# Performance work log

Hardware: AMD Instinct MI355X
Metric: run time of the kernel (lower is better)

The kernel has to match this reference:

```python
import jax, jax.numpy as jnp
import numpy as np

EMBED_DIM = 512
N_HEAD = 8
HEAD_DIM = EMBED_DIM // N_HEAD  # 64
B, S = 2, 4096
NEG_FILL = -1e20


def setup_inputs() -> dict:
    key = jax.random.key(0)
    ks = jax.random.split(key, 9)
    inp = {
        "key": jax.random.normal(ks[0], (B, S, EMBED_DIM), jnp.float32),
        "query": jax.random.normal(ks[1], (B, S, EMBED_DIM), jnp.float32),
        "value": jax.random.normal(ks[2], (B, S, EMBED_DIM), jnp.float32),
        "mask": jax.random.randint(ks[3], (1, 1, S, S), 0, 2, jnp.int32),
        # per-head projections (shared across heads, as in the source: a single
        # d x d nn.Linear applied to the last dim of [B,S,H,d])
        "Wq": jax.random.normal(ks[4], (HEAD_DIM, HEAD_DIM), jnp.float32) / np.sqrt(HEAD_DIM),
        "Wk": jax.random.normal(ks[5], (HEAD_DIM, HEAD_DIM), jnp.float32) / np.sqrt(HEAD_DIM),
        "Wv": jax.random.normal(ks[6], (HEAD_DIM, HEAD_DIM), jnp.float32) / np.sqrt(HEAD_DIM),
        "Wo": jax.random.normal(ks[7], (EMBED_DIM, EMBED_DIM), jnp.float32) / np.sqrt(EMBED_DIM),
        "bo": jax.random.normal(ks[8], (EMBED_DIM,), jnp.float32) * 0.01,
    }
    return inp


def reference(key, query, value, mask, Wq, Wk, Wv, Wo, bo):
    b, sq, e = query.shape
    skv = key.shape[1]
    h, d = N_HEAD, HEAD_DIM
    # split heads: [B, S, H, d]
    q = query.reshape(b, sq, h, d) @ Wq.T
    k = key.reshape(b, skv, h, d) @ Wk.T
    v = value.reshape(b, skv, h, d) @ Wv.T
    # scores: [B, H, Sq, Skv]
    scores = jnp.einsum("bqhd,bkhd->bhqk", q, k)
    # source masks BEFORE scaling: fill -1e20 then divide by sqrt(d)
    scores = jnp.where(mask == 0, NEG_FILL, scores)
    scores = scores / np.sqrt(d).astype(np.float32)
    attn = jax.nn.softmax(scores, axis=-1)
    ctx = jnp.einsum("bhqk,bkhd->bqhd", attn, v)  # [B, Sq, H, d]
    concat = ctx.reshape(b, sq, h * d)
    return concat @ Wo.T + bo
```

## Files before the change

kernel.cpp:

```cpp
#include <hip/hip_runtime.h>

typedef __bf16 bf16;
typedef __attribute__((ext_vector_type(8)))  bf16     bf16x8;
typedef __attribute__((ext_vector_type(4)))  bf16     bf16x4;
typedef __attribute__((ext_vector_type(16))) float    f32x16;
typedef __attribute__((ext_vector_type(4)))  float    f32x4;
typedef __attribute__((ext_vector_type(4)))  unsigned uint4v;
typedef __attribute__((ext_vector_type(2)))  unsigned uint2v;

#define SLEN 4096
#define NHEAD 8
#define HDIM 64
#define EMB 512
#define LOG2E 1.4426950408889634f
#define SCALE_LOG2E 0.1803336100254854f

__device__ __forceinline__ f32x16 mfma32(bf16x8 a, bf16x8 b, f32x16 c) {
  return __builtin_amdgcn_mfma_f32_32x32x16_bf16(a, b, c, 0, 0, 0);
}

__device__ __forceinline__ void cp16(const void* g, const void* l) {
  __builtin_amdgcn_global_load_lds(
      (__attribute__((address_space(1))) unsigned int*)(unsigned long long)g,
      (__attribute__((address_space(3))) unsigned int*)(unsigned int)(unsigned long long)l,
      16, 0, 0);
}

__device__ __forceinline__ unsigned pk2(float a, float b) {
  unsigned short ua = __builtin_bit_cast(unsigned short, (bf16)a);
  unsigned short ub = __builtin_bit_cast(unsigned short, (bf16)b);
  return (unsigned)ua | ((unsigned)ub << 16);
}

__global__ __launch_bounds__(256, 2) void proj_qkv(
    const float* __restrict__ key, const float* __restrict__ query, const float* __restrict__ value,
    const float* __restrict__ Wq, const float* __restrict__ Wk, const float* __restrict__ Wv,
    bf16* __restrict__ Qb, bf16* __restrict__ Kb, bf16* __restrict__ VT)
{
  __shared__ __align__(16) bf16 tile[128][64];
  const int tid = threadIdx.x, w = tid >> 6, lane = tid & 63, l31 = lane & 31, lh = lane >> 5;
  const int r0 = blockIdx.x * 128;
  const int m0 = r0 + w * 32;

  #pragma unroll
  for (int p = 0; p < 3; ++p) {
    const float* X = (p == 0) ? query : (p == 1) ? key : value;
    const float* W = (p == 0) ? Wq    : (p == 1) ? Wk  : Wv;

    bf16x8 af[4];
    {
      const float* xr = X + (size_t)(m0 + l31) * 64 + 8 * lh;
      #pragma unroll
      for (int c = 0; c < 4; ++c) {
        f32x4 lo = *(const f32x4*)(xr + c * 16);
        f32x4 hi = *(const f32x4*)(xr + c * 16 + 4);
        bf16x8 v;
        #pragma unroll
        for (int j = 0; j < 4; ++j) { v[j] = (bf16)lo[j]; v[4 + j] = (bf16)hi[j]; }
        af[c] = v;
      }
    }
    bf16x8 bfr[2][4];
    #pragma unroll
    for (int nb = 0; nb < 2; ++nb) {
      const float* wr = W + (size_t)(l31 + 32 * nb) * 64 + 8 * lh;
      #pragma unroll
      for (int c = 0; c < 4; ++c) {
        f32x4 lo = *(const f32x4*)(wr + c * 16);
        f32x4 hi = *(const f32x4*)(wr + c * 16 + 4);
        bf16x8 v;
        #pragma unroll
        for (int j = 0; j < 4; ++j) { v[j] = (bf16)lo[j]; v[4 + j] = (bf16)hi[j]; }
        bfr[nb][c] = v;
      }
    }
    f32x16 a0, a1;
    #pragma unroll
    for (int r = 0; r < 16; ++r) { a0[r] = 0.f; a1[r] = 0.f; }
    #pragma unroll
    for (int c = 0; c < 4; ++c) {
      a0 = mfma32(af[c], bfr[0][c], a0);
      a1 = mfma32(af[c], bfr[1][c], a1);
    }

    __syncthreads();
    #pragma unroll
    for (int r = 0; r < 16; ++r) {
      const int row = w * 32 + (r & 3) + 8 * (r >> 2) + 4 * lh;
      tile[row][l31]      = (bf16)a0[r];
      tile[row][l31 + 32] = (bf16)a1[r];
    }
    __syncthreads();

    if (p < 2) {
      bf16* OUT = p ? Kb : Qb;
      const int rloc = tid >> 1, half = tid & 1;
      const int rg = r0 + rloc, bs = rg >> 3, h = rg & 7, b = bs >> 12, sidx = bs & 4095;
      bf16* dst = OUT + (((size_t)(b * 8 + h) * SLEN + sidx) * 64 + half * 32);
      const bf16* srcp = &tile[rloc][half * 32];
      #pragma unroll
      for (int u = 0; u < 4; ++u) *(uint4v*)(dst + u * 8) = *(const uint4v*)(srcp + u * 8);
    } else {
      const int h = tid >> 5, d0 = tid & 31;
      const int b = blockIdx.x >> 8, s0 = (blockIdx.x * 16) & 4095;
      #pragma unroll
      for (int dh = 0; dh < 2; ++dh) {
        const int dd = d0 + 32 * dh;
        unsigned pk4[8];
        #pragma unroll
        for (int t2 = 0; t2 < 8; ++t2) {
          unsigned short ua = __builtin_bit_cast(unsigned short, tile[(2 * t2) * 8 + h][dd]);
          unsigned short ub = __builtin_bit_cast(unsigned short, tile[(2 * t2 + 1) * 8 + h][dd]);
          pk4[t2] = (unsigned)ua | ((unsigned)ub << 16);
        }
        bf16* dst = VT + ((size_t)(b * 8 + h) * 64 + dd) * SLEN + s0;
        uint4v A; A[0] = pk4[0]; A[1] = pk4[1]; A[2] = pk4[2]; A[3] = pk4[3];
        uint4v Bv; Bv[0] = pk4[4]; Bv[1] = pk4[5]; Bv[2] = pk4[6]; Bv[3] = pk4[7];
        *(uint4v*)(dst) = A;
        *(uint4v*)(dst + 8) = Bv;
      }
    }
  }
}

__global__ void pack_mask(const int* __restrict__ mask, unsigned long long* __restrict__ MBt)
{
  const int w = threadIdx.x >> 6, lane = threadIdx.x & 63;
  const int q = blockIdx.x * 4 + w;
  const int* row = mask + (size_t)q * SLEN;
  unsigned long long mine = 0ull;
  #pragma unroll 4
  for (int i = 0; i < 64; ++i) {
    unsigned long long b = __ballot(row[i * 64 + lane] != 0);
    if (i == lane) mine = b;
  }
  MBt[(size_t)lane * SLEN + q] = mine;
}

__global__ void wo_split(const float* __restrict__ Wo, bf16* __restrict__ WH, bf16* __restrict__ WL)
{
  const int i = (blockIdx.x * 256 + threadIdx.x) * 4;
  f32x4 v = *(const f32x4*)(Wo + i);
  bf16x4 h, l;
  #pragma unroll
  for (int j = 0; j < 4; ++j) { h[j] = (bf16)v[j]; l[j] = (bf16)(v[j] - (float)h[j]); }
  *(bf16x4*)(WH + i) = h;
  *(bf16x4*)(WL + i) = l;
}

__device__ __forceinline__ void stage_kv2(const bf16* Kb, const bf16* VT, bf16* Kf, bf16* Vf,
                                          int bh, int kv0, int buf, int w, int l31, int lh)
{
  #pragma unroll
  for (int qq = 0; qq < 4; ++qq) {
    const int fid = w * 4 + qq, mb = fid >> 2, c = fid & 3;
    const bf16* ks = Kb + ((size_t)bh * SLEN + kv0 + 32 * mb + l31) * HDIM + c * 16 + 8 * lh;
    cp16(ks, Kf + buf * 4096 + fid * 512);
    const bf16* vs = VT + ((size_t)bh * HDIM + 32 * mb + l31) * SLEN + kv0 + c * 16 + 8 * lh;
    cp16(vs, Vf + buf * 4096 + fid * 512);
  }
}

__global__ __launch_bounds__(128, 2) void attn_kernel(
    const bf16* __restrict__ Qb, const bf16* __restrict__ Kb, const bf16* __restrict__ VT,
    const unsigned long long* __restrict__ MBt,
    bf16* __restrict__ ctxh, bf16* __restrict__ ctxl)
{
  __shared__ __align__(16) unsigned char smem[32768];
  bf16* Kf = (bf16*)smem;
  bf16* Vf = (bf16*)(smem + 16384);

  const int tid = threadIdx.x, w = tid >> 6, lane = tid & 63, l31 = lane & 31, lh = lane >> 5;
  const int bh = blockIdx.x >> 6, qt = blockIdx.x & 63;
  const int q0 = qt * 64;
  const int qrow = q0 + w * 32 + l31;
  const int lh4 = 4 * lh;

  bf16x8 qf[4];
  {
    const bf16* qp = Qb + ((size_t)bh * SLEN + qrow) * HDIM + 8 * lh;
    #pragma unroll
    for (int c = 0; c < 4; ++c) qf[c] = *(const bf16x8*)(qp + c * 16);
  }

  f32x16 o0, o1;
  #pragma unroll
  for (int r = 0; r < 16; ++r) { o0[r] = 0.f; o1[r] = 0.f; }
  float ls0 = 0.f, ls1 = 0.f, ls2 = 0.f, ls3 = 0.f;

  stage_kv2(Kb, VT, Kf, Vf, bh, 0, 0, w, l31, lh);
  __syncthreads();

  unsigned long long mw = MBt[qrow];
  const int NT = SLEN / 64;
  for (int t = 0; t < NT; ++t) {
    const int cur = t & 1;
    if (t + 1 < NT) stage_kv2(Kb, VT, Kf, Vf, bh, (t + 1) * 64, cur ^ 1, w, l31, lh);
    unsigned long long mwn = 0ull;
    if (t + 1 < NT) mwn = MBt[(size_t)(t + 1) * SLEN + qrow];

    f32x16 s0, s1;
    #pragma unroll
    for (int r = 0; r < 16; ++r) { s0[r] = 0.f; s1[r] = 0.f; }
    #pragma unroll
    for (int c = 0; c < 4; ++c) {
      bf16x8 a0 = *(const bf16x8*)(Kf + cur * 4096 + c * 512 + lane * 8);
      bf16x8 a1 = *(const bf16x8*)(Kf + cur * 4096 + (4 + c) * 512 + lane * 8);
      s0 = mfma32(a0, qf[c], s0);
      s1 = mfma32(a1, qf[c], s1);
    }

    const unsigned wlo = (unsigned)mw, whi = (unsigned)(mw >> 32);
    float p0[16], p1[16];
    #pragma unroll
    for (int r = 0; r < 16; ++r) {
      const int sh = (r & 3) + 8 * (r >> 2) + lh4;
      float e0 = exp2f(s0[r] * SCALE_LOG2E);
      float e1 = exp2f(s1[r] * SCALE_LOG2E);
      e0 *= (float)((wlo >> sh) & 1u);
      e1 *= (float)((whi >> sh) & 1u);
      p0[r] = e0; p1[r] = e1;
      if ((r & 1) == 0) { ls0 += e0; ls1 += e1; } else { ls2 += e0; ls3 += e1; }
    }

    bf16x8 bp[4];
    #pragma unroll
    for (int mi = 0; mi < 2; ++mi) {
      #pragma unroll
      for (int cc = 0; cc < 2; ++cc) {
        const int rb = cc * 8;
        unsigned wA0 = pk2(mi ? p1[rb + 0] : p0[rb + 0], mi ? p1[rb + 1] : p0[rb + 1]);
        unsigned wA1 = pk2(mi ? p1[rb + 2] : p0[rb + 2], mi ? p1[rb + 3] : p0[rb + 3]);
        unsigned wB0 = pk2(mi ? p1[rb + 4] : p0[rb + 4], mi ? p1[rb + 5] : p0[rb + 5]);
        unsigned wB1 = pk2(mi ? p1[rb + 6] : p0[rb + 6], mi ? p1[rb + 7] : p0[rb + 7]);
        uint2v r0 = __builtin_amdgcn_permlane32_swap(wA0, wB0, false, false);
        uint2v r1 = __builtin_amdgcn_permlane32_swap(wA1, wB1, false, false);
        uint4v fw; fw[0] = r0[0]; fw[1] = r1[0]; fw[2] = r0[1]; fw[3] = r1[1];
        bp[2 * mi + cc] = __builtin_bit_cast(bf16x8, fw);
      }
    }

    #pragma unroll
    for (int c = 0; c < 4; ++c) {
      bf16x8 v0 = *(const bf16x8*)(Vf + cur * 4096 + c * 512 + lane * 8);
      bf16x8 v1 = *(const bf16x8*)(Vf + cur * 4096 + (4 + c) * 512 + lane * 8);
      o0 = mfma32(v0, bp[c], o0);
      o1 = mfma32(v1, bp[c], o1);
    }

    __syncthreads();
    mw = mwn;
  }

  float lsum = (ls0 + ls2) + (ls1 + ls3);
  lsum += __shfl_xor(lsum, 32);
  const float inv = 1.f / lsum;
  #pragma unroll
  for (int r = 0; r < 16; ++r) { o0[r] *= inv; o1[r] *= inv; }

  bf16* Tr = (bf16*)smem;
  const int rloc = tid >> 1, half = tid & 1;

  #pragma unroll
  for (int r = 0; r < 16; ++r) {
    const int dr = (r & 3) + 8 * (r >> 2) + lh4;
    Tr[(w * 32 + l31) * 72 + dr]      = (bf16)o0[r];
    Tr[(w * 32 + l31) * 72 + 32 + dr] = (bf16)o1[r];
  }
  __syncthreads();
  {
    bf16* dst = ctxh + ((size_t)bh * SLEN + q0 + rloc) * 64 + half * 32;
    const bf16* srcp = Tr + rloc * 72 + half * 32;
    #pragma unroll
    for (int u = 0; u < 4; ++u) *(uint4v*)(dst + u * 8) = *(const uint4v*)(srcp + u * 8);
  }
  __syncthreads();
  #pragma unroll
  for (int r = 0; r < 16; ++r) {
    const int dr = (r & 3) + 8 * (r >> 2) + lh4;
    const float h0 = (float)(bf16)o0[r];
    const float h1 = (float)(bf16)o1[r];
    Tr[(w * 32 + l31) * 72 + dr]      = (bf16)(o0[r] - h0);
    Tr[(w * 32 + l31) * 72 + 32 + dr] = (bf16)(o1[r] - h1);
  }
  __syncthreads();
  {
    bf16* dst = ctxl + ((size_t)bh * SLEN + q0 + rloc) * 64 + half * 32;
    const bf16* srcp = Tr + rloc * 72 + half * 32;
    #pragma unroll
    for (int u = 0; u < 4; ++u) *(uint4v*)(dst + u * 8) = *(const uint4v*)(srcp + u * 8);
  }
}

__global__ __launch_bounds__(256, 2) void out_proj(
    const bf16* __restrict__ CH, const bf16* __restrict__ CL,
    const bf16* __restrict__ WH, const bf16* __restrict__ WL,
    const float* __restrict__ bo, float* __restrict__ out)
{
  __shared__ __align__(16) bf16 Af[2][4][4][64][8];
  const int tid = threadIdx.x, w = tid >> 6, lane = tid & 63, l31 = lane & 31, lh = lane >> 5;
  const int mt = blockIdx.x >> 3, nt = blockIdx.x & 7;
  const int bs0 = mt * 128, n0 = nt * 64;
  const int b = bs0 >> 12, sbase = bs0 & 4095;

  f32x16 a0, a1;
  #pragma unroll
  for (int r = 0; r < 16; ++r) { a0[r] = 0.f; a1[r] = 0.f; }

  for (int kk = 0; kk < 8; ++kk) {
    __syncthreads();
    #pragma unroll
    for (int qq = 0; qq < 8; ++qq) {
      const int fid = w * 8 + qq, pl = fid >> 4, mb = (fid >> 2) & 3, c = fid & 3;
      const bf16* src = (pl ? CL : CH) +
          ((size_t)(b * 8 + kk) * SLEN + sbase + 32 * mb + l31) * 64 + 16 * c + 8 * lh;
      cp16(src, &Af[pl][mb][c][0][0]);
    }
    __syncthreads();

    bf16x8 bh0[4], bl0[4], bh1[4], bl1[4], ah[4], al[4];
    #pragma unroll
    for (int c = 0; c < 4; ++c) {
      const size_t o0off = (size_t)(n0 + l31) * EMB + kk * 64 + 16 * c + 8 * lh;
      const size_t o1off = (size_t)(n0 + l31 + 32) * EMB + kk * 64 + 16 * c + 8 * lh;
      bh0[c] = *(const bf16x8*)(WH + o0off);
      bl0[c] = *(const bf16x8*)(WL + o0off);
      bh1[c] = *(const bf16x8*)(WH + o1off);
      bl1[c] = *(const bf16x8*)(WL + o1off);
      ah[c] = *(const bf16x8*)(&Af[0][w][c][lane][0]);
      al[c] = *(const bf16x8*)(&Af[1][w][c][lane][0]);
    }
    #pragma unroll
    for (int c = 0; c < 4; ++c) {
      a0 = mfma32(ah[c], bh0[c], a0);
      a0 = mfma32(ah[c], bl0[c], a0);
      a0 = mfma32(al[c], bh0[c], a0);
      a1 = mfma32(ah[c], bh1[c], a1);
      a1 = mfma32(ah[c], bl1[c], a1);
      a1 = mfma32(al[c], bh1[c], a1);
    }
  }

  const float bv0 = bo[n0 + l31], bv1 = bo[n0 + l31 + 32];
  #pragma unroll
  for (int r = 0; r < 16; ++r) {
    const int row = bs0 + w * 32 + (r & 3) + 8 * (r >> 2) + 4 * lh;
    out[(size_t)row * EMB + n0 + l31]      = a0[r] + bv0;
    out[(size_t)row * EMB + n0 + l31 + 32] = a1[r] + bv1;
  }
}

extern "C" void kernel_launch(void* const* d_in, const int* in_sizes, int n_in,
                              void* d_out, int out_size, void* d_ws, size_t ws_size,
                              hipStream_t stream)
{
  (void)in_sizes; (void)n_in; (void)out_size; (void)ws_size;
  const float* key   = (const float*)d_in[0];
  const float* query = (const float*)d_in[1];
  const float* value = (const float*)d_in[2];
  const int*   mask  = (const int*)d_in[3];
  const float* Wq    = (const float*)d_in[4];
  const float* Wk    = (const float*)d_in[5];
  const float* Wv    = (const float*)d_in[6];
  const float* Wo    = (const float*)d_in[7];
  const float* bo    = (const float*)d_in[8];
  float* out = (float*)d_out;

  char* ws = (char*)d_ws;
  bf16* Qb = (bf16*)(ws);
  bf16* Kb = (bf16*)(ws + (8ull  << 20));
  bf16* VT = (bf16*)(ws + (16ull << 20));
  unsigned long long* MBp = (unsigned long long*)(ws + (24ull << 20));
  bf16* CH = (bf16*)(ws + (26ull << 20));
  bf16* CL = (bf16*)(ws + (34ull << 20));
  bf16* WH = (bf16*)(ws + (42ull << 20));
  bf16* WL = (bf16*)(ws + (42ull << 20) + (512ull << 10));

  proj_qkv<<<512, 256, 0, stream>>>(key, query, value, Wq, Wk, Wv, Qb, Kb, VT);
  pack_mask<<<1024, 256, 0, stream>>>(mask, MBp);
  wo_split<<<256, 256, 0, stream>>>(Wo, WH, WL);
  attn_kernel<<<1024, 128, 0, stream>>>(Qb, Kb, VT, MBp, CH, CL);
  out_proj<<<512, 256, 0, stream>>>(CH, CL, WH, WL, bo, out);
}
```

Measured before the change: 275.5 us.

## Split each KV tile across two extra waves per query group, reducing partials via LDS

The attention block grows from 2 to 4 waves. Each pair of waves handles one 32-row query group, and within the pair each wave takes half of every 64-key tile. Each wave now holds one score tile instead of two, which cuts its exp and packing work and register use per tile. The mask is repacked into two 32-bit words per 64-key tile, split by half-lane, so each wave can shift out its 16 mask bits directly. The trade-off is an extra LDS reduction of the partial outputs and softmax sums at the end. Occupancy is raised by using more waves per block.

```diff
diff --git a/kernel.cpp b/kernel.cpp
--- a/kernel.cpp
+++ b/kernel.cpp
@@ -12,7 +12,7 @@
 #define NHEAD 8
 #define HDIM 64
 #define EMB 512
-#define LOG2E 1.4426950408889634f
+#define NTILES 64
 #define SCALE_LOG2E 0.1803336100254854f
 
 __device__ __forceinline__ f32x16 mfma32(bf16x8 a, bf16x8 b, f32x16 c) {
@@ -123,7 +123,12 @@
   }
 }
 
-__global__ void pack_mask(const int* __restrict__ mask, unsigned long long* __restrict__ MBt)
+__device__ __forceinline__ unsigned nib_compress(unsigned x) {
+  x = (x | (x >> 4)) & 0x00FF00FFu;
+  x = (x | (x >> 8)) & 0x0000FFFFu;
+  return x;
+}
+__global__ void pack_mask(const int* __restrict__ mask, unsigned* __restrict__ MW)
 {
   const int w = threadIdx.x >> 6, lane = threadIdx.x & 63;
   const int q = blockIdx.x * 4 + w;
@@ -134,7 +139,11 @@
     unsigned long long b = __ballot(row[i * 64 + lane] != 0);
     if (i == lane) mine = b;
   }
-  MBt[(size_t)lane * SLEN + q] = mine;
+  const unsigned lo = (unsigned)mine, hi = (unsigned)(mine >> 32);
+  const unsigned w0 = nib_compress(lo & 0x0F0F0F0Fu)        | (nib_compress(hi & 0x0F0F0F0Fu) << 16);
+  const unsigned w1 = nib_compress((lo >> 4) & 0x0F0F0F0Fu) | (nib_compress((hi >> 4) & 0x0F0F0F0Fu) << 16);
+  MW[(size_t)lane * SLEN + q] = w0;
+  MW[(size_t)NTILES * SLEN + (size_t)lane * SLEN + q] = w1;
 }
 
 __global__ void wo_split(const float* __restrict__ Wo, bf16* __restrict__ WH, bf16* __restrict__ WL)
@@ -148,12 +157,12 @@
   *(bf16x4*)(WL + i) = l;
 }
 
-__device__ __forceinline__ void stage_kv2(const bf16* Kb, const bf16* VT, bf16* Kf, bf16* Vf,
+__device__ __forceinline__ void stage_kv4(const bf16* Kb, const bf16* VT, bf16* Kf, bf16* Vf,
                                           int bh, int kv0, int buf, int w, int l31, int lh)
 {
   #pragma unroll
-  for (int qq = 0; qq < 4; ++qq) {
-    const int fid = w * 4 + qq, mb = fid >> 2, c = fid & 3;
+  for (int qq = 0; qq < 2; ++qq) {
+    const int fid = w * 2 + qq, mb = fid >> 2, c = fid & 3;
     const bf16* ks = Kb + ((size_t)bh * SLEN + kv0 + 32 * mb + l31) * HDIM + c * 16 + 8 * lh;
     cp16(ks, Kf + buf * 4096 + fid * 512);
     const bf16* vs = VT + ((size_t)bh * HDIM + 32 * mb + l31) * SLEN + kv0 + c * 16 + 8 * lh;
@@ -161,9 +170,9 @@
   }
 }
 
-__global__ __launch_bounds__(128, 2) void attn_kernel(
+__global__ __launch_bounds__(256, 4) void attn_kernel(
     const bf16* __restrict__ Qb, const bf16* __restrict__ Kb, const bf16* __restrict__ VT,
-    const unsigned long long* __restrict__ MBt,
+    const unsigned* __restrict__ MW,
     bf16* __restrict__ ctxh, bf16* __restrict__ ctxl)
 {
   __shared__ __align__(16) unsigned char smem[32768];
@@ -171,9 +180,10 @@
   bf16* Vf = (bf16*)(smem + 16384);
 
   const int tid = threadIdx.x, w = tid >> 6, lane = tid & 63, l31 = lane & 31, lh = lane >> 5;
+  const int qg = w & 1, kc = w >> 1;
   const int bh = blockIdx.x >> 6, qt = blockIdx.x & 63;
   const int q0 = qt * 64;
-  const int qrow = q0 + w * 32 + l31;
+  const int qrow = q0 + qg * 32 + l31;
   const int lh4 = 4 * lh;
 
   bf16x8 qf[4];
@@ -188,103 +198,126 @@
   for (int r = 0; r < 16; ++r) { o0[r] = 0.f; o1[r] = 0.f; }
   float ls0 = 0.f, ls1 = 0.f, ls2 = 0.f, ls3 = 0.f;
 
-  stage_kv2(Kb, VT, Kf, Vf, bh, 0, 0, w, l31, lh);
-  __syncthreads();
-
-  unsigned long long mw = MBt[qrow];
-  const int NT = SLEN / 64;
-  for (int t = 0; t < NT; ++t) {
+  stage_kv4(Kb, VT, Kf, Vf, bh, 0, 0, w, l31, lh);
+  __syncthreads();
+
+  const unsigned* MWl = MW + (size_t)lh * NTILES * SLEN;
+  unsigned mw = MWl[qrow];
+  for (int t = 0; t < NTILES; ++t) {
     const int cur = t & 1;
-    if (t + 1 < NT) stage_kv2(Kb, VT, Kf, Vf, bh, (t + 1) * 64, cur ^ 1, w, l31, lh);
-    unsigned long long mwn = 0ull;
-    if (t + 1 < NT) mwn = MBt[(size_t)(t + 1) * SLEN + qrow];
-
-    f32x16 s0, s1;
-    #pragma unroll
-    for (int r = 0; r < 16; ++r) { s0[r] = 0.f; s1[r] = 0.f; }
+    if (t + 1 < NTILES) stage_kv4(Kb, VT, Kf, Vf, bh, (t + 1) * 64, cur ^ 1, w, l31, lh);
+    unsigned mwn = 0u;
+    if (t + 1 < NTILES) mwn = MWl[(size_t)(t + 1) * SLEN + qrow];
+
+    f32x16 s;
+    #pragma unroll
+    for (int r = 0; r < 16; ++r) s[r] = 0.f;
     #pragma unroll
     for (int c = 0; c < 4; ++c) {
-      bf16x8 a0 = *(const bf16x8*)(Kf + cur * 4096 + c * 512 + lane * 8);
-      bf16x8 a1 = *(const bf16x8*)(Kf + cur * 4096 + (4 + c) * 512 + lane * 8);
-      s0 = mfma32(a0, qf[c], s0);
-      s1 = mfma32(a1, qf[c], s1);
-    }
-
-    const unsigned wlo = (unsigned)mw, whi = (unsigned)(mw >> 32);
-    float p0[16], p1[16];
-    #pragma unroll
-    for (int r = 0; r < 16; ++r) {
-      const int sh = (r & 3) + 8 * (r >> 2) + lh4;
-      float e0 = exp2f(s0[r] * SCALE_LOG2E);
-      float e1 = exp2f(s1[r] * SCALE_LOG2E);
-      e0 *= (float)((wlo >> sh) & 1u);
-      e1 *= (float)((whi >> sh) & 1u);
-      p0[r] = e0; p1[r] = e1;
-      if ((r & 1) == 0) { ls0 += e0; ls1 += e1; } else { ls2 += e0; ls3 += e1; }
-    }
-
-    bf16x8 bp[4];
-    #pragma unroll
-    for (int mi = 0; mi < 2; ++mi) {
-      #pragma unroll
-      for (int cc = 0; cc < 2; ++cc) {
-        const int rb = cc * 8;
-        unsigned wA0 = pk2(mi ? p1[rb + 0] : p0[rb + 0], mi ? p1[rb + 1] : p0[rb + 1]);
-        unsigned wA1 = pk2(mi ? p1[rb + 2] : p0[rb + 2], mi ? p1[rb + 3] : p0[rb + 3]);
-        unsigned wB0 = pk2(mi ? p1[rb + 4] : p0[rb + 4], mi ? p1[rb + 5] : p0[rb + 5]);
-        unsigned wB1 = pk2(mi ? p1[rb + 6] : p0[rb + 6], mi ? p1[rb + 7] : p0[rb + 7]);
-        uint2v r0 = __builtin_amdgcn_permlane32_swap(wA0, wB0, false, false);
-        uint2v r1 = __builtin_amdgcn_permlane32_swap(wA1, wB1, false, false);
-        uint4v fw; fw[0] = r0[0]; fw[1] = r1[0]; fw[2] = r0[1]; fw[3] = r1[1];
-        bp[2 * mi + cc] = __builtin_bit_cast(bf16x8, fw);
-      }
-    }
-
-    #pragma unroll
-    for (int c = 0; c < 4; ++c) {
-      bf16x8 v0 = *(const bf16x8*)(Vf + cur * 4096 + c * 512 + lane * 8);
-      bf16x8 v1 = *(const bf16x8*)(Vf + cur * 4096 + (4 + c) * 512 + lane * 8);
-      o0 = mfma32(v0, bp[c], o0);
-      o1 = mfma32(v1, bp[c], o1);
+      bf16x8 a = *(const bf16x8*)(Kf + cur * 4096 + (kc * 4 + c) * 512 + lane * 8);
+      s = mfma32(a, qf[c], s);
+    }
+
+    const unsigned mwk = mw >> (kc * 16);
+    float p[16];
+    #pragma unroll
+    for (int r = 0; r < 16; ++r) {
+      float e = __builtin_amdgcn_exp2f(s[r] * SCALE_LOG2E);
+      e *= (float)((mwk >> r) & 1u);
+      p[r] = e;
+      if      ((r & 3) == 0) ls0 += e;
+      else if ((r & 3) == 1) ls1 += e;
+      else if ((r & 3) == 2) ls2 += e;
+      else                   ls3 += e;
+    }
+
+    bf16x8 bp[2];
+    #pragma unroll
+    for (int cc = 0; cc < 2; ++cc) {
+      const int rb = cc * 8;
+      unsigned wA0 = pk2(p[rb + 0], p[rb + 1]);
+      unsigned wA1 = pk2(p[rb + 2], p[rb + 3]);
+      unsigned wB0 = pk2(p[rb + 4], p[rb + 5]);
+      unsigned wB1 = pk2(p[rb + 6], p[rb + 7]);
+      uint2v r0 = __builtin_amdgcn_permlane32_swap(wA0, wB0, false, false);
+      uint2v r1 = __builtin_amdgcn_permlane32_swap(wA1, wB1, false, false);
+      uint4v fw; fw[0] = r0[0]; fw[1] = r1[0]; fw[2] = r0[1]; fw[3] = r1[1];
+      bp[cc] = __builtin_bit_cast(bf16x8, fw);
+    }
+
+    #pragma unroll
+    for (int cc = 0; cc < 2; ++cc) {
+      bf16x8 v0 = *(const bf16x8*)(Vf + cur * 4096 + (0 * 4 + kc * 2 + cc) * 512 + lane * 8);
+      bf16x8 v1 = *(const bf16x8*)(Vf + cur * 4096 + (1 * 4 + kc * 2 + cc) * 512 + lane * 8);
+      o0 = mfma32(v0, bp[cc], o0);
+      o1 = mfma32(v1, bp[cc], o1);
     }
 
     __syncthreads();
     mw = mwn;
   }
 
-  float lsum = (ls0 + ls2) + (ls1 + ls3);
-  lsum += __shfl_xor(lsum, 32);
-  const float inv = 1.f / lsum;
-  #pragma unroll
-  for (int r = 0; r < 16; ++r) { o0[r] *= inv; o1[r] *= inv; }
-
-  bf16* Tr = (bf16*)smem;
-  const int rloc = tid >> 1, half = tid & 1;
-
-  #pragma unroll
-  for (int r = 0; r < 16; ++r) {
-    const int dr = (r & 3) + 8 * (r >> 2) + lh4;
-    Tr[(w * 32 + l31) * 72 + dr]      = (bf16)o0[r];
-    Tr[(w * 32 + l31) * 72 + 32 + dr] = (bf16)o1[r];
-  }
-  __syncthreads();
-  {
+  float plsum = (ls0 + ls1) + (ls2 + ls3);
+  plsum += __shfl_xor(plsum, 32);
+
+  float* PO = (float*)smem;
+  float* PL = (float*)(smem + 16384);
+  bf16*  Tr = (bf16*)(smem + 17408);
+
+  if (w >= 2) {
+    const int pw = w - 2;
+    #pragma unroll
+    for (int r = 0; r < 16; ++r) {
+      PO[(pw * 32 + r) * 64 + lane]      = o0[r];
+      PO[(pw * 32 + 16 + r) * 64 + lane] = o1[r];
+    }
+    PL[pw * 64 + lane] = plsum;
+  }
+  __syncthreads();
+
+  if (w < 2) {
+    #pragma unroll
+    for (int r = 0; r < 16; ++r) {
+      o0[r] += PO[(w * 32 + r) * 64 + lane];
+      o1[r] += PO[(w * 32 + 16 + r) * 64 + lane];
+    }
+    plsum += PL[w * 64 + lane];
+    const float inv = 1.f / plsum;
+    #pragma unroll
+    for (int r = 0; r < 16; ++r) { o0[r] *= inv; o1[r] *= inv; }
+  }
+  __syncthreads();
+
+  if (w < 2) {
+    #pragma unroll
+    for (int r = 0; r < 16; ++r) {
+      const int dr = (r & 3) + 8 * (r >> 2) + lh4;
+      Tr[(w * 32 + l31) * 72 + dr]      = (bf16)o0[r];
+      Tr[(w * 32 + l31) * 72 + 32 + dr] = (bf16)o1[r];
+    }
+  }
+  __syncthreads();
+  if (tid < 128) {
+    const int rloc = tid >> 1, half = tid & 1;
     bf16* dst = ctxh + ((size_t)bh * SLEN + q0 + rloc) * 64 + half * 32;
     const bf16* srcp = Tr + rloc * 72 + half * 32;
     #pragma unroll
     for (int u = 0; u < 4; ++u) *(uint4v*)(dst + u * 8) = *(const uint4v*)(srcp + u * 8);
   }
   __syncthreads();
-  #pragma unroll
-  for (int r = 0; r < 16; ++r) {
-    const int dr = (r & 3) + 8 * (r >> 2) + lh4;
-    const float h0 = (float)(bf16)o0[r];
-    const float h1 = (float)(bf16)o1[r];
-    Tr[(w * 32 + l31) * 72 + dr]      = (bf16)(o0[r] - h0);
-    Tr[(w * 32 + l31) * 72 + 32 + dr] = (bf16)(o1[r] - h1);
-  }
-  __syncthreads();
-  {
+  if (w < 2) {
+    #pragma unroll
+    for (int r = 0; r < 16; ++r) {
+      const int dr = (r & 3) + 8 * (r >> 2) + lh4;
+      const float h0 = (float)(bf16)o0[r];
+      const float h1 = (float)(bf16)o1[r];
+      Tr[(w * 32 + l31) * 72 + dr]      = (bf16)(o0[r] - h0);
+      Tr[(w * 32 + l31) * 72 + 32 + dr] = (bf16)(o1[r] - h1);
+    }
+  }
+  __syncthreads();
+  if (tid < 128) {
+    const int rloc = tid >> 1, half = tid & 1;
     bf16* dst = ctxl + ((size_t)bh * SLEN + q0 + rloc) * 64 + half * 32;
     const bf16* srcp = Tr + rloc * 72 + half * 32;
     #pragma unroll
@@ -370,15 +403,15 @@
   bf16* Qb = (bf16*)(ws);
   bf16* Kb = (bf16*)(ws + (8ull  << 20));
   bf16* VT = (bf16*)(ws + (16ull << 20));
-  unsigned long long* MBp = (unsigned long long*)(ws + (24ull << 20));
+  unsigned* MW = (unsigned*)(ws + (24ull << 20));
   bf16* CH = (bf16*)(ws + (26ull << 20));
   bf16* CL = (bf16*)(ws + (34ull << 20));
   bf16* WH = (bf16*)(ws + (42ull << 20));
   bf16* WL = (bf16*)(ws + (42ull << 20) + (512ull << 10));
 
   proj_qkv<<<512, 256, 0, stream>>>(key, query, value, Wq, Wk, Wv, Qb, Kb, VT);
-  pack_mask<<<1024, 256, 0, stream>>>(mask, MBp);
+  pack_mask<<<1024, 256, 0, stream>>>(mask, MW);
   wo_split<<<256, 256, 0, stream>>>(Wo, WH, WL);
-  attn_kernel<<<1024, 128, 0, stream>>>(Qb, Kb, VT, MBp, CH, CL);
+  attn_kernel<<<1024, 256, 0, stream>>>(Qb, Kb, VT, MW, CH, CL);
   out_proj<<<512, 256, 0, stream>>>(CH, CL, WH, WL, bo, out);
 }
```

New measurement: 233.8 us. -15.1%, faster.

## Restructure attention to 16x16 MFMA tiles with 4 waves and repacked mask

Applied to the files above, without the earlier changes.

The attention kernel now uses 256 threads per block, with each wave owning 16 query rows, and computes with 16x16x32 bf16 MFMAs instead of 32x32. Probabilities are moved into B-operand layout with ds_bpermute, and masking uses a bitwise AND instead of a multiply. The softmax scale is folded into the Q projection, and the mask is repacked into a per-lane byte layout to suit the new fragment mapping. This is meant to raise occupancy, cut per-element VALU work and shorten the epilogue, at the cost of more LDS permute traffic and smaller MFMA tiles.

```diff
diff --git a/kernel.cpp b/kernel.cpp
--- a/kernel.cpp
+++ b/kernel.cpp
@@ -9,14 +9,15 @@
 typedef __attribute__((ext_vector_type(2)))  unsigned uint2v;
 
 #define SLEN 4096
-#define NHEAD 8
 #define HDIM 64
 #define EMB 512
-#define LOG2E 1.4426950408889634f
 #define SCALE_LOG2E 0.1803336100254854f
 
 __device__ __forceinline__ f32x16 mfma32(bf16x8 a, bf16x8 b, f32x16 c) {
   return __builtin_amdgcn_mfma_f32_32x32x16_bf16(a, b, c, 0, 0, 0);
+}
+__device__ __forceinline__ f32x4 mfma16(bf16x8 a, bf16x8 b, f32x4 c) {
+  return __builtin_amdgcn_mfma_f32_16x16x32_bf16(a, b, c, 0, 0, 0);
 }
 
 __device__ __forceinline__ void cp16(const void* g, const void* l) {
@@ -83,12 +84,13 @@
       a1 = mfma32(af[c], bfr[1][c], a1);
     }
 
+    const float qs = (p == 0) ? SCALE_LOG2E : 1.0f;
     __syncthreads();
     #pragma unroll
     for (int r = 0; r < 16; ++r) {
       const int row = w * 32 + (r & 3) + 8 * (r >> 2) + 4 * lh;
-      tile[row][l31]      = (bf16)a0[r];
-      tile[row][l31 + 32] = (bf16)a1[r];
+      tile[row][l31]      = (bf16)(a0[r] * qs);
+      tile[row][l31 + 32] = (bf16)(a1[r] * qs);
     }
     __syncthreads();
 
@@ -123,7 +125,7 @@
   }
 }
 
-__global__ void pack_mask(const int* __restrict__ mask, unsigned long long* __restrict__ MBt)
+__global__ void pack_mask(const int* __restrict__ mask, unsigned char* __restrict__ MW4)
 {
   const int w = threadIdx.x >> 6, lane = threadIdx.x & 63;
   const int q = blockIdx.x * 4 + w;
@@ -134,7 +136,14 @@
     unsigned long long b = __ballot(row[i * 64 + lane] != 0);
     if (i == lane) mine = b;
   }
-  MBt[(size_t)lane * SLEN + q] = mine;
+  const unsigned lo = (unsigned)mine, hi = (unsigned)(mine >> 32);
+  #pragma unroll
+  for (int gg = 0; gg < 4; ++gg) {
+    unsigned b0 = ((lo >> (4 * gg)) & 0xFu) | (((lo >> (16 + 4 * gg)) & 0xFu) << 4);
+    unsigned b1 = ((hi >> (4 * gg)) & 0xFu) | (((hi >> (16 + 4 * gg)) & 0xFu) << 4);
+    *(unsigned short*)(MW4 + ((size_t)gg * 4096 + q) * 128 + 2 * lane) =
+        (unsigned short)(b0 | (b1 << 8));
+  }
 }
 
 __global__ void wo_split(const float* __restrict__ Wo, bf16* __restrict__ WH, bf16* __restrict__ WL)
@@ -148,148 +157,168 @@
   *(bf16x4*)(WL + i) = l;
 }
 
-__device__ __forceinline__ void stage_kv2(const bf16* Kb, const bf16* VT, bf16* Kf, bf16* Vf,
-                                          int bh, int kv0, int buf, int w, int l31, int lh)
-{
-  #pragma unroll
-  for (int qq = 0; qq < 4; ++qq) {
-    const int fid = w * 4 + qq, mb = fid >> 2, c = fid & 3;
-    const bf16* ks = Kb + ((size_t)bh * SLEN + kv0 + 32 * mb + l31) * HDIM + c * 16 + 8 * lh;
-    cp16(ks, Kf + buf * 4096 + fid * 512);
-    const bf16* vs = VT + ((size_t)bh * HDIM + 32 * mb + l31) * SLEN + kv0 + c * 16 + 8 * lh;
-    cp16(vs, Vf + buf * 4096 + fid * 512);
-  }
-}
-
-__global__ __launch_bounds__(128, 2) void attn_kernel(
+__global__ __launch_bounds__(256, 4) void attn_kernel(
     const bf16* __restrict__ Qb, const bf16* __restrict__ Kb, const bf16* __restrict__ VT,
-    const unsigned long long* __restrict__ MBt,
+    const unsigned char* __restrict__ MW4,
     bf16* __restrict__ ctxh, bf16* __restrict__ ctxl)
 {
   __shared__ __align__(16) unsigned char smem[32768];
-  bf16* Kf = (bf16*)smem;
-  bf16* Vf = (bf16*)(smem + 16384);
-
-  const int tid = threadIdx.x, w = tid >> 6, lane = tid & 63, l31 = lane & 31, lh = lane >> 5;
-  const int bh = blockIdx.x >> 6, qt = blockIdx.x & 63;
-  const int q0 = qt * 64;
-  const int qrow = q0 + w * 32 + l31;
-  const int lh4 = 4 * lh;
-
-  bf16x8 qf[4];
-  {
-    const bf16* qp = Qb + ((size_t)bh * SLEN + qrow) * HDIM + 8 * lh;
-    #pragma unroll
-    for (int c = 0; c < 4; ++c) qf[c] = *(const bf16x8*)(qp + c * 16);
-  }
-
-  f32x16 o0, o1;
-  #pragma unroll
-  for (int r = 0; r < 16; ++r) { o0[r] = 0.f; o1[r] = 0.f; }
-  float ls0 = 0.f, ls1 = 0.f, ls2 = 0.f, ls3 = 0.f;
-
-  stage_kv2(Kb, VT, Kf, Vf, bh, 0, 0, w, l31, lh);
+  unsigned char* const Ksm = smem;
+  unsigned char* const Vsm = smem + 16384;
+
+  const int tid = threadIdx.x, w = tid >> 6, lane = tid & 63;
+  const int g = lane >> 4, q15 = lane & 15;
+  const int bh = blockIdx.x >> 6;
+  const int q0w = (blockIdx.x & 63) * 64 + w * 16;
+
+  const bf16* qp = Qb + ((size_t)bh * SLEN + q0w + q15) * HDIM + 8 * g;
+  const bf16x8 qf0 = *(const bf16x8*)(qp);
+  const bf16x8 qf1 = *(const bf16x8*)(qp + 32);
+
+  const int fk0 = 2 * w, fk1 = 2 * w + 1;
+  const bf16* kp0 = Kb + ((size_t)bh * SLEN + (fk0 >> 2) * 32 + ((fk0 >> 1) & 1) * 16 + q15) * HDIM
+                       + (fk0 & 1) * 32 + 8 * g;
+  const bf16* kp1 = Kb + ((size_t)bh * SLEN + (fk1 >> 2) * 32 + ((fk1 >> 1) & 1) * 16 + q15) * HDIM
+                       + (fk1 & 1) * 32 + 8 * g;
+  const bf16* vp0 = VT + ((size_t)(bh * 64 + (fk0 & 3) * 16 + q15)) * SLEN + (fk0 >> 2) * 32 + 8 * g;
+  const bf16* vp1 = VT + ((size_t)(bh * 64 + (fk1 & 3) * 16 + q15)) * SLEN + (fk1 >> 2) * 32 + 8 * g;
+
+  unsigned char* const dK0a = Ksm + fk0 * 1024;
+  unsigned char* const dK1a = Ksm + fk1 * 1024;
+  unsigned char* const dK0b = Ksm + 8192 + fk0 * 1024;
+  unsigned char* const dK1b = Ksm + 8192 + fk1 * 1024;
+  unsigned char* const dV0a = Vsm + fk0 * 1024;
+  unsigned char* const dV1a = Vsm + fk1 * 1024;
+  unsigned char* const dV0b = Vsm + 8192 + fk0 * 1024;
+  unsigned char* const dV1b = Vsm + 8192 + fk1 * 1024;
+
+  f32x4 o0 = {0.f, 0.f, 0.f, 0.f}, o1 = o0, o2 = o0, o3 = o0;
+  const f32x4 Z4 = {0.f, 0.f, 0.f, 0.f};
+  float la0 = 0.f, la1 = 0.f, la2 = 0.f, la3 = 0.f;
+
+  const int idx0 = (32 * (g & 1) + q15) * 4;
+  const int idx1 = idx0 + 64;
+  const bool bhi = (g >= 2);
+
+  const unsigned char* mp = MW4 + ((size_t)g * 4096 + q0w + q15) * 128;
+  unsigned mw = *(const unsigned*)(mp);
+
+  cp16(kp0, dK0a); cp16(kp1, dK1a); cp16(vp0, dV0a); cp16(vp1, dV1a);
+  kp0 += 4096; kp1 += 4096; vp0 += 64; vp1 += 64;
   __syncthreads();
 
-  unsigned long long mw = MBt[qrow];
-  const int NT = SLEN / 64;
-  for (int t = 0; t < NT; ++t) {
-    const int cur = t & 1;
-    if (t + 1 < NT) stage_kv2(Kb, VT, Kf, Vf, bh, (t + 1) * 64, cur ^ 1, w, l31, lh);
-    unsigned long long mwn = 0ull;
-    if (t + 1 < NT) mwn = MBt[(size_t)(t + 1) * SLEN + qrow];
-
-    f32x16 s0, s1;
-    #pragma unroll
-    for (int r = 0; r < 16; ++r) { s0[r] = 0.f; s1[r] = 0.f; }
-    #pragma unroll
-    for (int c = 0; c < 4; ++c) {
-      bf16x8 a0 = *(const bf16x8*)(Kf + cur * 4096 + c * 512 + lane * 8);
-      bf16x8 a1 = *(const bf16x8*)(Kf + cur * 4096 + (4 + c) * 512 + lane * 8);
-      s0 = mfma32(a0, qf[c], s0);
-      s1 = mfma32(a1, qf[c], s1);
-    }
-
-    const unsigned wlo = (unsigned)mw, whi = (unsigned)(mw >> 32);
-    float p0[16], p1[16];
-    #pragma unroll
-    for (int r = 0; r < 16; ++r) {
-      const int sh = (r & 3) + 8 * (r >> 2) + lh4;
-      float e0 = exp2f(s0[r] * SCALE_LOG2E);
-      float e1 = exp2f(s1[r] * SCALE_LOG2E);
-      e0 *= (float)((wlo >> sh) & 1u);
-      e1 *= (float)((whi >> sh) & 1u);
-      p0[r] = e0; p1[r] = e1;
-      if ((r & 1) == 0) { ls0 += e0; ls1 += e1; } else { ls2 += e0; ls3 += e1; }
-    }
-
-    bf16x8 bp[4];
-    #pragma unroll
-    for (int mi = 0; mi < 2; ++mi) {
-      #pragma unroll
-      for (int cc = 0; cc < 2; ++cc) {
-        const int rb = cc * 8;
-        unsigned wA0 = pk2(mi ? p1[rb + 0] : p0[rb + 0], mi ? p1[rb + 1] : p0[rb + 1]);
-        unsigned wA1 = pk2(mi ? p1[rb + 2] : p0[rb + 2], mi ? p1[rb + 3] : p0[rb + 3]);
-        unsigned wB0 = pk2(mi ? p1[rb + 4] : p0[rb + 4], mi ? p1[rb + 5] : p0[rb + 5]);
-        unsigned wB1 = pk2(mi ? p1[rb + 6] : p0[rb + 6], mi ? p1[rb + 7] : p0[rb + 7]);
-        uint2v r0 = __builtin_amdgcn_permlane32_swap(wA0, wB0, false, false);
-        uint2v r1 = __builtin_amdgcn_permlane32_swap(wA1, wB1, false, false);
-        uint4v fw; fw[0] = r0[0]; fw[1] = r1[0]; fw[2] = r0[1]; fw[3] = r1[1];
-        bp[2 * mi + cc] = __builtin_bit_cast(bf16x8, fw);
-      }
-    }
-
-    #pragma unroll
-    for (int c = 0; c < 4; ++c) {
-      bf16x8 v0 = *(const bf16x8*)(Vf + cur * 4096 + c * 512 + lane * 8);
-      bf16x8 v1 = *(const bf16x8*)(Vf + cur * 4096 + (4 + c) * 512 + lane * 8);
-      o0 = mfma32(v0, bp[c], o0);
-      o1 = mfma32(v1, bp[c], o1);
-    }
-
-    __syncthreads();
-    mw = mwn;
-  }
-
-  float lsum = (ls0 + ls2) + (ls1 + ls3);
+  const int lb = lane * 16;
+
+#define LDK(BUF, U, BLK, C) \
+  (*(const bf16x8*)(Ksm + (BUF) * 8192 + (((U) * 4 + (BLK) * 2 + (C)) * 1024) + lb))
+#define LDV(BUF, U, DB) \
+  (*(const bf16x8*)(Vsm + (BUF) * 8192 + (((U) * 4 + (DB)) * 1024) + lb))
+
+#define MEXP(dst, sv, POS) { \
+  float e_ = __builtin_amdgcn_exp2f(sv); \
+  unsigned k_ = (unsigned)(((int)(mw << (31 - (POS)))) >> 31); \
+  dst = __builtin_bit_cast(float, __builtin_bit_cast(unsigned, e_) & k_); }
+
+#define SUBSTEP(BUF, U, BYTE) { \
+  f32x4 sb0 = mfma16(LDK(BUF, U, 0, 0), qf0, Z4); \
+  sb0 = mfma16(LDK(BUF, U, 0, 1), qf1, sb0); \
+  f32x4 sb1 = mfma16(LDK(BUF, U, 1, 0), qf0, Z4); \
+  sb1 = mfma16(LDK(BUF, U, 1, 1), qf1, sb1); \
+  float p00, p01, p02, p03, p10, p11, p12, p13; \
+  MEXP(p00, sb0[0], 8 * (BYTE) + 0) MEXP(p01, sb0[1], 8 * (BYTE) + 1) \
+  MEXP(p02, sb0[2], 8 * (BYTE) + 2) MEXP(p03, sb0[3], 8 * (BYTE) + 3) \
+  MEXP(p10, sb1[0], 8 * (BYTE) + 4) MEXP(p11, sb1[1], 8 * (BYTE) + 5) \
+  MEXP(p12, sb1[2], 8 * (BYTE) + 6) MEXP(p13, sb1[3], 8 * (BYTE) + 7) \
+  la0 += p00 + p10; la1 += p01 + p11; la2 += p02 + p12; la3 += p03 + p13; \
+  const unsigned W00 = pk2(p00, p01), W01 = pk2(p02, p03); \
+  const unsigned W10 = pk2(p10, p11), W11 = pk2(p12, p13); \
+  const unsigned a00 = (unsigned)__builtin_amdgcn_ds_bpermute(idx0, (int)W00); \
+  const unsigned a10 = (unsigned)__builtin_amdgcn_ds_bpermute(idx0, (int)W10); \
+  const unsigned a01 = (unsigned)__builtin_amdgcn_ds_bpermute(idx0, (int)W01); \
+  const unsigned a11 = (unsigned)__builtin_amdgcn_ds_bpermute(idx0, (int)W11); \
+  const unsigned b00 = (unsigned)__builtin_amdgcn_ds_bpermute(idx1, (int)W00); \
+  const unsigned b10 = (unsigned)__builtin_amdgcn_ds_bpermute(idx1, (int)W10); \
+  const unsigned b01 = (unsigned)__builtin_amdgcn_ds_bpermute(idx1, (int)W01); \
+  const unsigned b11 = (unsigned)__builtin_amdgcn_ds_bpermute(idx1, (int)W11); \
+  uint4v fw; \
+  fw[0] = bhi ? a10 : a00;  fw[1] = bhi ? a11 : a01; \
+  fw[2] = bhi ? b10 : b00;  fw[3] = bhi ? b11 : b01; \
+  const bf16x8 bp = __builtin_bit_cast(bf16x8, fw); \
+  o0 = mfma16(LDV(BUF, U, 0), bp, o0); o1 = mfma16(LDV(BUF, U, 1), bp, o1); \
+  o2 = mfma16(LDV(BUF, U, 2), bp, o2); o3 = mfma16(LDV(BUF, U, 3), bp, o3); \
+}
+
+#define TILE(BUF, BYTE, DK0, DK1, DV0, DV1) { \
+  cp16(kp0, DK0); cp16(kp1, DK1); cp16(vp0, DV0); cp16(vp1, DV1); \
+  kp0 += 4096; kp1 += 4096; vp0 += 64; vp1 += 64; \
+  SUBSTEP(BUF, 0, (BYTE)) \
+  SUBSTEP(BUF, 1, (BYTE) + 1) \
+  __syncthreads(); \
+}
+
+  for (int tp = 0; tp < 32; ++tp) {
+    const unsigned mwn = *(const unsigned*)(mp + 4);
+    TILE(0, 0, dK0b, dK1b, dV0b, dV1b)
+    TILE(1, 2, dK0a, dK1a, dV0a, dV1a)
+    mw = mwn; mp += 4;
+  }
+
+  float lsum = (la0 + la1) + (la2 + la3);
+  lsum += __shfl_xor(lsum, 16);
   lsum += __shfl_xor(lsum, 32);
   const float inv = 1.f / lsum;
   #pragma unroll
-  for (int r = 0; r < 16; ++r) { o0[r] *= inv; o1[r] *= inv; }
-
-  bf16* Tr = (bf16*)smem;
-  const int rloc = tid >> 1, half = tid & 1;
-
-  #pragma unroll
-  for (int r = 0; r < 16; ++r) {
-    const int dr = (r & 3) + 8 * (r >> 2) + lh4;
-    Tr[(w * 32 + l31) * 72 + dr]      = (bf16)o0[r];
-    Tr[(w * 32 + l31) * 72 + 32 + dr] = (bf16)o1[r];
-  }
+  for (int r = 0; r < 4; ++r) { o0[r] *= inv; o1[r] *= inv; o2[r] *= inv; o3[r] *= inv; }
+
   __syncthreads();
+  unsigned char* const Tr = smem + w * 4096;
+  const int trw = q15 * 136 + 8 * g;
+  const int qq = lane >> 2, part = lane & 3;
+  const int rb = qq * 136 + part * 32;
+  bf16* dsth = ctxh + ((size_t)bh * SLEN + q0w + qq) * HDIM + part * 16;
+  bf16* dstl = ctxl + ((size_t)bh * SLEN + q0w + qq) * HDIM + part * 16;
+
+  { uint2v t; t[0] = pk2(o0[0], o0[1]); t[1] = pk2(o0[2], o0[3]); *(uint2v*)(Tr + trw)      = t; }
+  { uint2v t; t[0] = pk2(o1[0], o1[1]); t[1] = pk2(o1[2], o1[3]); *(uint2v*)(Tr + trw + 32) = t; }
+  { uint2v t; t[0] = pk2(o2[0], o2[1]); t[1] = pk2(o2[2], o2[3]); *(uint2v*)(Tr + trw + 64) = t; }
+  { uint2v t; t[0] = pk2(o3[0], o3[1]); t[1] = pk2(o3[2], o3[3]); *(uint2v*)(Tr + trw + 96) = t; }
   {
-    bf16* dst = ctxh + ((size_t)bh * SLEN + q0 + rloc) * 64 + half * 32;
-    const bf16* srcp = Tr + rloc * 72 + half * 32;
-    #pragma unroll
-    for (int u = 0; u < 4; ++u) *(uint4v*)(dst + u * 8) = *(const uint4v*)(srcp + u * 8);
-  }
-  __syncthreads();
-  #pragma unroll
-  for (int r = 0; r < 16; ++r) {
-    const int dr = (r & 3) + 8 * (r >> 2) + lh4;
-    const float h0 = (float)(bf16)o0[r];
-    const float h1 = (float)(bf16)o1[r];
-    Tr[(w * 32 + l31) * 72 + dr]      = (bf16)(o0[r] - h0);
-    Tr[(w * 32 + l31) * 72 + 32 + dr] = (bf16)(o1[r] - h1);
-  }
-  __syncthreads();
+    uint2v r0 = *(const uint2v*)(Tr + rb);
+    uint2v r1 = *(const uint2v*)(Tr + rb + 8);
+    uint2v r2 = *(const uint2v*)(Tr + rb + 16);
+    uint2v r3 = *(const uint2v*)(Tr + rb + 24);
+    uint4v s0; s0[0] = r0[0]; s0[1] = r0[1]; s0[2] = r1[0]; s0[3] = r1[1];
+    uint4v s1; s1[0] = r2[0]; s1[1] = r2[1]; s1[2] = r3[0]; s1[3] = r3[1];
+    *(uint4v*)(dsth) = s0;
+    *(uint4v*)(dsth + 8) = s1;
+  }
+  f32x4 l0, l1, l2, l3;
+  #pragma unroll
+  for (int r = 0; r < 4; ++r) {
+    l0[r] = o0[r] - (float)(bf16)o0[r];
+    l1[r] = o1[r] - (float)(bf16)o1[r];
+    l2[r] = o2[r] - (float)(bf16)o2[r];
+    l3[r] = o3[r] - (float)(bf16)o3[r];
+  }
+  { uint2v t; t[0] = pk2(l0[0], l0[1]); t[1] = pk2(l0[2], l0[3]); *(uint2v*)(Tr + trw)      = t; }
+  { uint2v t; t[0] = pk2(l1[0], l1[1]); t[1] = pk2(l1[2], l1[3]); *(uint2v*)(Tr + trw + 32) = t; }
+  { uint2v t; t[0] = pk2(l2[0], l2[1]); t[1] = pk2(l2[2], l2[3]); *(uint2v*)(Tr + trw + 64) = t; }
+  { uint2v t; t[0] = pk2(l3[0], l3[1]); t[1] = pk2(l3[2], l3[3]); *(uint2v*)(Tr + trw + 96) = t; }
   {
-    bf16* dst = ctxl + ((size_t)bh * SLEN + q0 + rloc) * 64 + half * 32;
-    const bf16* srcp = Tr + rloc * 72 + half * 32;
-    #pragma unroll
-    for (int u = 0; u < 4; ++u) *(uint4v*)(dst + u * 8) = *(const uint4v*)(srcp + u * 8);
-  }
+    uint2v r0 = *(const uint2v*)(Tr + rb);
+    uint2v r1 = *(const uint2v*)(Tr + rb + 8);
+    uint2v r2 = *(const uint2v*)(Tr + rb + 16);
+    uint2v r3 = *(const uint2v*)(Tr + rb + 24);
+    uint4v s0; s0[0] = r0[0]; s0[1] = r0[1]; s0[2] = r1[0]; s0[3] = r1[1];
+    uint4v s1; s1[0] = r2[0]; s1[1] = r2[1]; s1[2] = r3[0]; s1[3] = r3[1];
+    *(uint4v*)(dstl) = s0;
+    *(uint4v*)(dstl + 8) = s1;
+  }
+#undef LDK
+#undef LDV
+#undef MEXP
+#undef SUBSTEP
+#undef TILE
 }
 
 __global__ __launch_bounds__(256, 2) void out_proj(
@@ -370,15 +399,15 @@
   bf16* Qb = (bf16*)(ws);
   bf16* Kb = (bf16*)(ws + (8ull  << 20));
   bf16* VT = (bf16*)(ws + (16ull << 20));
-  unsigned long long* MBp = (unsigned long long*)(ws + (24ull << 20));
+  unsigned char* MW4 = (unsigned char*)(ws + (24ull << 20));
   bf16* CH = (bf16*)(ws + (26ull << 20));
   bf16* CL = (bf16*)(ws + (34ull << 20));
   bf16* WH = (bf16*)(ws + (42ull << 20));
   bf16* WL = (bf16*)(ws + (42ull << 20) + (512ull << 10));
 
   proj_qkv<<<512, 256, 0, stream>>>(key, query, value, Wq, Wk, Wv, Qb, Kb, VT);
-  pack_mask<<<1024, 256, 0, stream>>>(mask, MBp);
+  pack_mask<<<1024, 256, 0, stream>>>(mask, MW4);
   wo_split<<<256, 256, 0, stream>>>(Wo, WH, WL);
-  attn_kernel<<<1024, 128, 0, stream>>>(Qb, Kb, VT, MBp, CH, CL);
+  attn_kernel<<<1024, 256, 0, stream>>>(Qb, Kb, VT, MW4, CH, CL);
   out_proj<<<512, 256, 0, stream>>>(CH, CL, WH, WL, bo, out);
 }
```

New measurement: 244.0 us. 11.4% less time.
